# Kernel optimization log

Hardware: AMD Instinct MI355X
Metric: run time of the kernel (lower is better)

Reference implementation:

```python
import jax, jax.numpy as jnp
import numpy as np

N_NODES = 100000


def gcn_conv(x, edge_index, W, b):
    """PyG GCNConv: h = x @ W; out = D^-1/2 (A+I) D^-1/2 h + b."""
    n = x.shape[0]
    src, dst = edge_index[0], edge_index[1]
    loop = jnp.arange(n)
    src = jnp.concatenate([src, loop])  # add self-loops
    dst = jnp.concatenate([dst, loop])
    # degree at target nodes (unit edge weights)
    deg = jax.ops.segment_sum(jnp.ones(dst.shape[0], dtype=x.dtype), dst, num_segments=n)
    dinv = jnp.where(deg > 0, jax.lax.rsqrt(deg), 0.0)
    norm = dinv[src] * dinv[dst]  # [E+n]
    h = x @ W  # [n, out]
    msg = h[src] * norm[:, None]  # gather + scale
    out = jax.ops.segment_sum(msg, dst, num_segments=n)  # scatter-add
    return out + b


def setup_inputs() -> dict:
    key = jax.random.key(0)
    k1, k2, k3, k4, k5, k6 = jax.random.split(key, 6)
    E = 3200000
    x = jax.random.normal(k1, (N_NODES, 2), dtype=jnp.float32)
    edge_index = jax.random.randint(k2, (2, E), 0, N_NODES, dtype=jnp.int64)
    W1 = jax.random.normal(k3, (2, 16), dtype=jnp.float32) * 0.5
    b1 = jax.random.normal(k4, (16,), dtype=jnp.float32) * 0.1
    W2 = jax.random.normal(k5, (16, 2), dtype=jnp.float32) * 0.25
    b2 = jax.random.normal(k6, (2,), dtype=jnp.float32) * 0.1
    return {"x": x, "edge_index": edge_index, "W1": W1, "b1": b1, "W2": W2, "b2": b2}


def reference(x, edge_index, W1, b1, W2, b2):
    h = jax.nn.relu(gcn_conv(x, edge_index, W1, b1))
    # dropout is identity at inference
    out = gcn_conv(h, edge_index, W2, b2)
    return jax.nn.log_softmax(out, axis=1)
```

## Files before the change

### kernel.cpp

```cpp
#include <hip/hip_runtime.h>
#include <math.h>


constexpr int N = 100000;
constexpr int LOGB = 6;
constexpr int BNODES = 1 << LOGB;
constexpr int K = (N + BNODES - 1) / BNODES;
constexpr int KF = 49 * 32;
constexpr int CAPF = 2560;
constexpr int NC = 49;
constexpr int CAP1 = 68608;
constexpr int BSP = 512;
constexpr int ECHUNK = 8192;
constexpr int EPT = ECHUNK / BSP;
constexpr int MAXCH = 9;

__global__ __launch_bounds__(BSP) void k_pass1(const int* __restrict__ src,
                                               const int* __restrict__ dst, int E,
                                               int* __restrict__ gfill1,
                                               int* __restrict__ slotsC) {
    __shared__ int hist[NC];
    __shared__ int base[NC];
    int t = threadIdx.x;
    if (t < NC) hist[t] = 0;
    __syncthreads();
    int s[EPT], d[EPT];
    int ebase = blockIdx.x * ECHUNK + t * EPT;
#pragma unroll
    for (int k = 0; k < EPT / 4; k++) {
        int idx = ebase + 4 * k;
        if (idx + 3 < E) {
            *(int4*)(s + 4 * k) = *(const int4*)(src + idx);
            *(int4*)(d + 4 * k) = *(const int4*)(dst + idx);
        } else {
            for (int j = 0; j < 4; j++) {
                s[4 * k + j] = (idx + j < E) ? src[idx + j] : -1;
                d[4 * k + j] = (idx + j < E) ? dst[idx + j] : -1;
            }
        }
    }
#pragma unroll
    for (int k = 0; k < EPT; k++)
        if (d[k] >= 0) atomicAdd(&hist[d[k] >> 11], 1);
    __syncthreads();
    if (t < NC) {
        int c = hist[t];
        base[t] = c ? atomicAdd(&gfill1[t], c) : 0;
        hist[t] = 0;
    }
    __syncthreads();
#pragma unroll
    for (int k = 0; k < EPT; k++) {
        if (d[k] >= 0) {
            int bin = d[k] >> 11;
            int r = atomicAdd(&hist[bin], 1);
            int pos = base[bin] + r;
            if (pos < CAP1) slotsC[bin * CAP1 + pos] = (s[k] << 11) | (d[k] & 2047);
        }
    }
}

__global__ __launch_bounds__(BSP) void k_pass2(const int* __restrict__ gfill1,
                                               const int* __restrict__ slotsC,
                                               int* __restrict__ gfillF,
                                               int* __restrict__ slotsF) {
    __shared__ int hist[32];
    __shared__ int base[32];
    int c = blockIdx.x / MAXCH;
    int j = blockIdx.x % MAXCH;
    int fill = min(gfill1[c], CAP1);
    int e0 = j * ECHUNK;
    if (e0 >= fill) return;
    int e1 = min(fill, e0 + ECHUNK);
    int t = threadIdx.x;
    if (t < 32) hist[t] = 0;
    __syncthreads();
    const int* row = slotsC + c * CAP1;
    int v[EPT];
    int ebase = e0 + t * EPT;
#pragma unroll
    for (int k = 0; k < EPT / 4; k++) {
        int idx = ebase + 4 * k;
        if (idx + 3 < e1) {
            *(int4*)(v + 4 * k) = *(const int4*)(row + idx);
        } else {
            for (int jj = 0; jj < 4; jj++) v[4 * k + jj] = (idx + jj < e1) ? row[idx + jj] : -1;
        }
    }
#pragma unroll
    for (int k = 0; k < EPT; k++)
        if (v[k] >= 0) atomicAdd(&hist[(v[k] >> 6) & 31], 1);
    __syncthreads();
    if (t < 32) {
        int cc = hist[t];
        base[t] = cc ? atomicAdd(&gfillF[c * 32 + t], cc) : 0;
        hist[t] = 0;
    }
    __syncthreads();
#pragma unroll
    for (int k = 0; k < EPT; k++) {
        if (v[k] >= 0) {
            int b = (v[k] >> 6) & 31;
            int r = atomicAdd(&hist[b], 1);
            int pos = base[b] + r;
            if (pos < CAPF)
                slotsF[(c * 32 + b) * CAPF + pos] = ((v[k] >> 11) << 6) | (v[k] & 63);
        }
    }
}

__global__ __launch_bounds__(512) void k_degree(const int* __restrict__ gfillF,
                                                const int* __restrict__ slotsF,
                                                const float* __restrict__ x,
                                                float* __restrict__ dinv,
                                                float2* __restrict__ sx) {
    __shared__ int cnt[BNODES];
    int b = blockIdx.x, t = threadIdx.x;
    if (t < BNODES) cnt[t] = 0;
    __syncthreads();
    int count = min(gfillF[b], CAPF);
    const int* row = slotsF + b * CAPF;
    int nvec = count & ~3;
    for (int j = 4 * t; j < nvec; j += 4 * 512) {
        int4 p = *(const int4*)(row + j);
        atomicAdd(&cnt[p.x & (BNODES - 1)], 1);
        atomicAdd(&cnt[p.y & (BNODES - 1)], 1);
        atomicAdd(&cnt[p.z & (BNODES - 1)], 1);
        atomicAdd(&cnt[p.w & (BNODES - 1)], 1);
    }
    for (int j = nvec + t; j < count; j += 512) atomicAdd(&cnt[row[j] & (BNODES - 1)], 1);
    __syncthreads();
    if (t < BNODES) {
        int node = b * BNODES + t;
        if (node < N) {
            float di = rsqrtf((float)(cnt[t] + 1));
            dinv[node] = di;
            float2 xv = ((const float2*)x)[node];
            sx[node] = make_float2(xv.x * di, xv.y * di);
        }
    }
}

__global__ __launch_bounds__(512) void k_agg1(const int* __restrict__ gfillF,
                                              const int* __restrict__ slotsF,
                                              const float* __restrict__ dinv,
                                              const float2* __restrict__ sx,
                                              const float* __restrict__ W1,
                                              const float* __restrict__ b1,
                                              const float* __restrict__ W2,
                                              float2* __restrict__ sz) {
    __shared__ float accX[BNODES], accY[BNODES];
    __shared__ float sW1[32], sb1[16], sW2[32];
    int t = threadIdx.x;
    if (t < 32) sW1[t] = W1[t];
    if (t >= 32 && t < 48) sb1[t - 32] = b1[t - 32];
    if (t >= 48 && t < 80) sW2[t - 48] = W2[t - 48];
    if (t < BNODES) { accX[t] = 0.f; accY[t] = 0.f; }
    __syncthreads();
    int b = blockIdx.x;
    int count = min(gfillF[b], CAPF);
    const int* row = slotsF + b * CAPF;
    int nvec = count & ~3;
    for (int j = 4 * t; j < nvec; j += 4 * 512) {
        int4 p = *(const int4*)(row + j);
        float2 v0 = sx[p.x >> LOGB], v1 = sx[p.y >> LOGB];
        float2 v2 = sx[p.z >> LOGB], v3 = sx[p.w >> LOGB];
        atomicAdd(&accX[p.x & (BNODES - 1)], v0.x);
        atomicAdd(&accY[p.x & (BNODES - 1)], v0.y);
        atomicAdd(&accX[p.y & (BNODES - 1)], v1.x);
        atomicAdd(&accY[p.y & (BNODES - 1)], v1.y);
        atomicAdd(&accX[p.z & (BNODES - 1)], v2.x);
        atomicAdd(&accY[p.z & (BNODES - 1)], v2.y);
        atomicAdd(&accX[p.w & (BNODES - 1)], v3.x);
        atomicAdd(&accY[p.w & (BNODES - 1)], v3.y);
    }
    for (int j = nvec + t; j < count; j += 512) {
        int p = row[j];
        float2 v = sx[p >> LOGB];
        atomicAdd(&accX[p & (BNODES - 1)], v.x);
        atomicAdd(&accY[p & (BNODES - 1)], v.y);
    }
    __syncthreads();
    if (t < BNODES) {
        int node = b * BNODES + t;
        if (node < N) {
            float di = dinv[node];
            float2 sv = sx[node];
            float a0 = (accX[t] + sv.x) * di;
            float a1 = (accY[t] + sv.y) * di;
            float z0 = 0.f, z1 = 0.f;
#pragma unroll
            for (int k = 0; k < 16; k++) {
                float h = fmaf(a0, sW1[k], fmaf(a1, sW1[16 + k], sb1[k]));
                h = fmaxf(h, 0.f);
                z0 = fmaf(h, sW2[2 * k + 0], z0);
                z1 = fmaf(h, sW2[2 * k + 1], z1);
            }
            sz[node] = make_float2(z0 * di, z1 * di);
        }
    }
}

__global__ __launch_bounds__(512) void k_agg2(const int* __restrict__ gfillF,
                                              const int* __restrict__ slotsF,
                                              const float* __restrict__ dinv,
                                              const float2* __restrict__ sz,
                                              const float* __restrict__ b2,
                                              float2* __restrict__ out) {
    __shared__ float accX[BNODES], accY[BNODES];
    int b = blockIdx.x, t = threadIdx.x;
    if (t < BNODES) { accX[t] = 0.f; accY[t] = 0.f; }
    __syncthreads();
    int count = min(gfillF[b], CAPF);
    const int* row = slotsF + b * CAPF;
    int nvec = count & ~3;
    for (int j = 4 * t; j < nvec; j += 4 * 512) {
        int4 p = *(const int4*)(row + j);
        float2 v0 = sz[p.x >> LOGB], v1 = sz[p.y >> LOGB];
        float2 v2 = sz[p.z >> LOGB], v3 = sz[p.w >> LOGB];
        atomicAdd(&accX[p.x & (BNODES - 1)], v0.x);
        atomicAdd(&accY[p.x & (BNODES - 1)], v0.y);
        atomicAdd(&accX[p.y & (BNODES - 1)], v1.x);
        atomicAdd(&accY[p.y & (BNODES - 1)], v1.y);
        atomicAdd(&accX[p.z & (BNODES - 1)], v2.x);
        atomicAdd(&accY[p.z & (BNODES - 1)], v2.y);
        atomicAdd(&accX[p.w & (BNODES - 1)], v3.x);
        atomicAdd(&accY[p.w & (BNODES - 1)], v3.y);
    }
    for (int j = nvec + t; j < count; j += 512) {
        int p = row[j];
        float2 v = sz[p >> LOGB];
        atomicAdd(&accX[p & (BNODES - 1)], v.x);
        atomicAdd(&accY[p & (BNODES - 1)], v.y);
    }
    __syncthreads();
    if (t < BNODES) {
        int node = b * BNODES + t;
        if (node < N) {
            float di = dinv[node];
            float2 sv = sz[node];
            float v0 = fmaf(accX[t] + sv.x, di, b2[0]);
            float v1 = fmaf(accY[t] + sv.y, di, b2[1]);
            float m = fmaxf(v0, v1);
            float lse = m + logf(expf(v0 - m) + expf(v1 - m));
            out[node] = make_float2(v0 - lse, v1 - lse);
        }
    }
}

extern "C" void kernel_launch(void* const* d_in, const int* in_sizes, int n_in,
                              void* d_out, int out_size, void* d_ws, size_t ws_size,
                              hipStream_t stream) {
    const float* x  = (const float*)d_in[0];
    const int*   ei = (const int*)d_in[1];
    const float* W1 = (const float*)d_in[2];
    const float* b1 = (const float*)d_in[3];
    const float* W2 = (const float*)d_in[4];
    const float* b2 = (const float*)d_in[5];

    const int E = in_sizes[1] / 2;
    const int* src = ei;
    const int* dst = ei + E;
    const int GP = (E + ECHUNK - 1) / ECHUNK;

    char* ws = (char*)d_ws;
    size_t off = 0;
    auto alloc = [&](size_t bytes) {
        char* p = ws + off;
        off += (bytes + 511) & ~size_t(511);
        return p;
    };
    int*    fills  = (int*)alloc((NC + KF) * sizeof(int));
    float*  dinv   = (float*)alloc(N * sizeof(float));
    float2* sx     = (float2*)alloc(N * sizeof(float2));
    float2* sz     = (float2*)alloc(N * sizeof(float2));
    int*    slotsC = (int*)alloc((size_t)NC * CAP1 * sizeof(int));
    int*    slotsF = (int*)alloc((size_t)KF * CAPF * sizeof(int));
    int* gfill1 = fills;
    int* gfillF = fills + NC;

    hipMemsetAsync(fills, 0, (NC + KF) * sizeof(int), stream);

    k_pass1<<<GP, BSP, 0, stream>>>(src, dst, E, gfill1, slotsC);
    k_pass2<<<NC * MAXCH, BSP, 0, stream>>>(gfill1, slotsC, gfillF, slotsF);
    k_degree<<<K, 512, 0, stream>>>(gfillF, slotsF, x, dinv, sx);
    k_agg1<<<K, 512, 0, stream>>>(gfillF, slotsF, dinv, sx, W1, b1, W2, sz);
    k_agg2<<<K, 512, 0, stream>>>(gfillF, slotsF, dinv, sz, b2, (float2*)d_out);
}
```

Before: 202.5 us.

## Fold degree counting into pass2 and shrink aggregation block size

```diff
diff --git a/kernel.cpp b/kernel.cpp
--- a/kernel.cpp
+++ b/kernel.cpp
@@ -14,6 +14,7 @@
 constexpr int ECHUNK = 8192;
 constexpr int EPT = ECHUNK / BSP;
 constexpr int MAXCH = 9;
+constexpr int BAGG = 256;
 
 __global__ __launch_bounds__(BSP) void k_pass1(const int* __restrict__ src,
                                                const int* __restrict__ dst, int E,
@@ -63,17 +64,24 @@
 __global__ __launch_bounds__(BSP) void k_pass2(const int* __restrict__ gfill1,
                                                const int* __restrict__ slotsC,
                                                int* __restrict__ gfillF,
-                                               int* __restrict__ slotsF) {
+                                               int* __restrict__ slotsF,
+                                               int* __restrict__ degPart) {
     __shared__ int hist[32];
     __shared__ int base[32];
+    __shared__ int dh[2048];
     int c = blockIdx.x / MAXCH;
     int j = blockIdx.x % MAXCH;
     int fill = min(gfill1[c], CAP1);
     int e0 = j * ECHUNK;
-    if (e0 >= fill) return;
+    int t = threadIdx.x;
+    int* dpRow = degPart + blockIdx.x * 2048;
+    if (e0 >= fill) {
+        for (int i = t; i < 2048; i += BSP) dpRow[i] = 0;
+        return;
+    }
     int e1 = min(fill, e0 + ECHUNK);
-    int t = threadIdx.x;
     if (t < 32) hist[t] = 0;
+    for (int i = t; i < 2048; i += BSP) dh[i] = 0;
     __syncthreads();
     const int* row = slotsC + c * CAP1;
     int v[EPT];
@@ -89,7 +97,10 @@
     }
 #pragma unroll
     for (int k = 0; k < EPT; k++)
-        if (v[k] >= 0) atomicAdd(&hist[(v[k] >> 6) & 31], 1);
+        if (v[k] >= 0) {
+            atomicAdd(&hist[(v[k] >> 6) & 31], 1);
+            atomicAdd(&dh[v[k] & 2047], 1);
+        }
     __syncthreads();
     if (t < 32) {
         int cc = hist[t];
@@ -107,48 +118,34 @@
                 slotsF[(c * 32 + b) * CAPF + pos] = ((v[k] >> 11) << 6) | (v[k] & 63);
         }
     }
-}
-
-__global__ __launch_bounds__(512) void k_degree(const int* __restrict__ gfillF,
-                                                const int* __restrict__ slotsF,
-                                                const float* __restrict__ x,
-                                                float* __restrict__ dinv,
-                                                float2* __restrict__ sx) {
-    __shared__ int cnt[BNODES];
-    int b = blockIdx.x, t = threadIdx.x;
-    if (t < BNODES) cnt[t] = 0;
-    __syncthreads();
-    int count = min(gfillF[b], CAPF);
-    const int* row = slotsF + b * CAPF;
-    int nvec = count & ~3;
-    for (int j = 4 * t; j < nvec; j += 4 * 512) {
-        int4 p = *(const int4*)(row + j);
-        atomicAdd(&cnt[p.x & (BNODES - 1)], 1);
-        atomicAdd(&cnt[p.y & (BNODES - 1)], 1);
-        atomicAdd(&cnt[p.z & (BNODES - 1)], 1);
-        atomicAdd(&cnt[p.w & (BNODES - 1)], 1);
-    }
-    for (int j = nvec + t; j < count; j += 512) atomicAdd(&cnt[row[j] & (BNODES - 1)], 1);
-    __syncthreads();
-    if (t < BNODES) {
-        int node = b * BNODES + t;
-        if (node < N) {
-            float di = rsqrtf((float)(cnt[t] + 1));
-            dinv[node] = di;
-            float2 xv = ((const float2*)x)[node];
-            sx[node] = make_float2(xv.x * di, xv.y * di);
-        }
-    }
-}
-
-__global__ __launch_bounds__(512) void k_agg1(const int* __restrict__ gfillF,
-                                              const int* __restrict__ slotsF,
-                                              const float* __restrict__ dinv,
-                                              const float2* __restrict__ sx,
-                                              const float* __restrict__ W1,
-                                              const float* __restrict__ b1,
-                                              const float* __restrict__ W2,
-                                              float2* __restrict__ sz) {
+    for (int i = t; i < 2048; i += BSP) dpRow[i] = dh[i];
+}
+
+__global__ __launch_bounds__(BAGG) void k_dinv(const int* __restrict__ degPart,
+                                               const float* __restrict__ x,
+                                               float* __restrict__ dinv,
+                                               float2* __restrict__ sx) {
+    int node = blockIdx.x * BAGG + threadIdx.x;
+    if (node >= N) return;
+    int c = node >> 11, i = node & 2047;
+    const int* p = degPart + (size_t)c * MAXCH * 2048 + i;
+    int deg = 0;
+#pragma unroll
+    for (int j = 0; j < MAXCH; j++) deg += p[j * 2048];
+    float di = rsqrtf((float)(deg + 1));
+    dinv[node] = di;
+    float2 xv = ((const float2*)x)[node];
+    sx[node] = make_float2(xv.x * di, xv.y * di);
+}
+
+__global__ __launch_bounds__(BAGG) void k_agg1(const int* __restrict__ gfillF,
+                                               const int* __restrict__ slotsF,
+                                               const float* __restrict__ dinv,
+                                               const float2* __restrict__ sx,
+                                               const float* __restrict__ W1,
+                                               const float* __restrict__ b1,
+                                               const float* __restrict__ W2,
+                                               float2* __restrict__ sz) {
     __shared__ float accX[BNODES], accY[BNODES];
     __shared__ float sW1[32], sb1[16], sW2[32];
     int t = threadIdx.x;
@@ -161,7 +158,7 @@
     int count = min(gfillF[b], CAPF);
     const int* row = slotsF + b * CAPF;
     int nvec = count & ~3;
-    for (int j = 4 * t; j < nvec; j += 4 * 512) {
+    for (int j = 4 * t; j < nvec; j += 4 * BAGG) {
         int4 p = *(const int4*)(row + j);
         float2 v0 = sx[p.x >> LOGB], v1 = sx[p.y >> LOGB];
         float2 v2 = sx[p.z >> LOGB], v3 = sx[p.w >> LOGB];
@@ -174,7 +171,7 @@
         atomicAdd(&accX[p.w & (BNODES - 1)], v3.x);
         atomicAdd(&accY[p.w & (BNODES - 1)], v3.y);
     }
-    for (int j = nvec + t; j < count; j += 512) {
+    for (int j = nvec + t; j < count; j += BAGG) {
         int p = row[j];
         float2 v = sx[p >> LOGB];
         atomicAdd(&accX[p & (BNODES - 1)], v.x);
@@ -201,12 +198,12 @@
     }
 }
 
-__global__ __launch_bounds__(512) void k_agg2(const int* __restrict__ gfillF,
-                                              const int* __restrict__ slotsF,
-                                              const float* __restrict__ dinv,
-                                              const float2* __restrict__ sz,
-                                              const float* __restrict__ b2,
-                                              float2* __restrict__ out) {
+__global__ __launch_bounds__(BAGG) void k_agg2(const int* __restrict__ gfillF,
+                                               const int* __restrict__ slotsF,
+                                               const float* __restrict__ dinv,
+                                               const float2* __restrict__ sz,
+                                               const float* __restrict__ b2,
+                                               float2* __restrict__ out) {
     __shared__ float accX[BNODES], accY[BNODES];
     int b = blockIdx.x, t = threadIdx.x;
     if (t < BNODES) { accX[t] = 0.f; accY[t] = 0.f; }
@@ -214,7 +211,7 @@
     int count = min(gfillF[b], CAPF);
     const int* row = slotsF + b * CAPF;
     int nvec = count & ~3;
-    for (int j = 4 * t; j < nvec; j += 4 * 512) {
+    for (int j = 4 * t; j < nvec; j += 4 * BAGG) {
         int4 p = *(const int4*)(row + j);
         float2 v0 = sz[p.x >> LOGB], v1 = sz[p.y >> LOGB];
         float2 v2 = sz[p.z >> LOGB], v3 = sz[p.w >> LOGB];
@@ -227,7 +224,7 @@
         atomicAdd(&accX[p.w & (BNODES - 1)], v3.x);
         atomicAdd(&accY[p.w & (BNODES - 1)], v3.y);
     }
-    for (int j = nvec + t; j < count; j += 512) {
+    for (int j = nvec + t; j < count; j += BAGG) {
         int p = row[j];
         float2 v = sz[p >> LOGB];
         atomicAdd(&accX[p & (BNODES - 1)], v.x);
@@ -270,20 +267,21 @@
         off += (bytes + 511) & ~size_t(511);
         return p;
     };
-    int*    fills  = (int*)alloc((NC + KF) * sizeof(int));
-    float*  dinv   = (float*)alloc(N * sizeof(float));
-    float2* sx     = (float2*)alloc(N * sizeof(float2));
-    float2* sz     = (float2*)alloc(N * sizeof(float2));
-    int*    slotsC = (int*)alloc((size_t)NC * CAP1 * sizeof(int));
-    int*    slotsF = (int*)alloc((size_t)KF * CAPF * sizeof(int));
+    int*    fills   = (int*)alloc((NC + KF) * sizeof(int));
+    float*  dinv    = (float*)alloc(N * sizeof(float));
+    float2* sx      = (float2*)alloc(N * sizeof(float2));
+    float2* sz      = (float2*)alloc(N * sizeof(float2));
+    int*    slotsC  = (int*)alloc((size_t)NC * CAP1 * sizeof(int));
+    int*    slotsF  = (int*)alloc((size_t)KF * CAPF * sizeof(int));
+    int*    degPart = (int*)alloc((size_t)NC * MAXCH * 2048 * sizeof(int));
     int* gfill1 = fills;
     int* gfillF = fills + NC;
 
     hipMemsetAsync(fills, 0, (NC + KF) * sizeof(int), stream);
 
     k_pass1<<<GP, BSP, 0, stream>>>(src, dst, E, gfill1, slotsC);
-    k_pass2<<<NC * MAXCH, BSP, 0, stream>>>(gfill1, slotsC, gfillF, slotsF);
-    k_degree<<<K, 512, 0, stream>>>(gfillF, slotsF, x, dinv, sx);
-    k_agg1<<<K, 512, 0, stream>>>(gfillF, slotsF, dinv, sx, W1, b1, W2, sz);
-    k_agg2<<<K, 512, 0, stream>>>(gfillF, slotsF, dinv, sz, b2, (float2*)d_out);
-}
+    k_pass2<<<NC * MAXCH, BSP, 0, stream>>>(gfill1, slotsC, gfillF, slotsF, degPart);
+    k_dinv<<<(N + BAGG - 1) / BAGG, BAGG, 0, stream>>>(degPart, x, dinv, sx);
+    k_agg1<<<K, BAGG, 0, stream>>>(gfillF, slotsF, dinv, sx, W1, b1, W2, sz);
+    k_agg2<<<K, BAGG, 0, stream>>>(gfillF, slotsF, dinv, sz, b2, (float2*)d_out);
+}
```

After: 199.6 us. About the same (-1.4%).
